# Kernel optimization log

Measured on AMD Instinct MI355X. Metric: run time of the kernel, lower is better.

The kernel has to match this reference:

```python
import jax, jax.numpy as jnp
import numpy as np

T = 464
H = 256  # 256 * network_scale**2 with network_scale=1


def setup_inputs() -> dict:
    key = jax.random.key(0)
    ks = jax.random.split(key, 8)
    B = 64
    feature_encoded = jax.random.normal(ks[0], (B, T, H), dtype=jnp.float32)
    memory_state = jax.random.normal(ks[1], (B, H), dtype=jnp.float32) * 0.1
    carry_state = jax.random.normal(ks[2], (B, H), dtype=jnp.float32) * 0.1
    # LSTM params: kernel [H, 4H], recurrent kernel [H, 4H], bias [4H]; gate order i,f,c,o (Keras)
    # small init scale keeps the relu-activated recurrence numerically stable over 464 steps
    W = jax.random.normal(ks[3], (H, 4 * H), dtype=jnp.float32) * 0.02
    U = jax.random.normal(ks[4], (H, 4 * H), dtype=jnp.float32) * 0.02
    b = jnp.zeros((4 * H,), dtype=jnp.float32)
    # trailing dense: Flatten([B, T, H]) -> Dense(H, relu)
    Wd = jax.random.normal(ks[5], (T * H, H), dtype=jnp.float32) * (1.0 / np.sqrt(T * H))
    bd = jnp.zeros((H,), dtype=jnp.float32)
    return {"feature_encoded": feature_encoded, "memory_state": memory_state,
            "carry_state": carry_state, "W": W, "U": U, "b": b, "Wd": Wd, "bd": bd}


def _lstm_relu(x, h0, c0, W, U, b):
    # Keras LSTM with activation='relu', recurrent_activation='sigmoid'.
    def step(carry, x_t):
        h, c = carry
        z = x_t @ W + h @ U + b           # [B, 4H]
        zi, zf, zg, zo = jnp.split(z, 4, axis=-1)
        i = jax.nn.sigmoid(zi)
        f = jax.nn.sigmoid(zf)
        c = f * c + i * jax.nn.relu(zg)
        o = jax.nn.sigmoid(zo)
        h = o * jax.nn.relu(c)
        return (h, c), h

    xs = jnp.swapaxes(x, 0, 1)            # [T, B, H]
    (hT, cT), ys = jax.lax.scan(step, (h0, c0), xs)
    return jnp.swapaxes(ys, 0, 1), hT, cT  # [B, T, H], [B, H], [B, H]


def reference(feature_encoded, memory_state, carry_state, W, U, b, Wd, bd):
    B = feature_encoded.shape[0]
    x = feature_encoded.reshape(B, T, H)
    seq, hT, cT = _lstm_relu(x, memory_state, carry_state, W, U, b)
    flat = seq.reshape(B, T * H)
    core_output = jax.nn.relu(flat @ Wd + bd)  # [B, H]
    return core_output, hT, cT
```

## Files before the change

### kernel.cpp

```cpp
#include <hip/hip_runtime.h>

#define TT  464
#define HH  256
#define BB  64
#define NWG 64

using bf16x8 = __attribute__((ext_vector_type(8))) short;
using f32x4  = __attribute__((ext_vector_type(4))) float;

__device__ __forceinline__ unsigned short f2bf(float x) {
  union { float f; unsigned u; } v; v.f = x;
  unsigned r = v.u + 0x7fffu + ((v.u >> 16) & 1u);
  return (unsigned short)(r >> 16);
}

__device__ __forceinline__ void wait_flags(int* flags, int base, int target) {
  const int ln  = threadIdx.x & 63;
  int* p = &flags[base + (ln & 31)];
  for (;;) {
    int f = __hip_atomic_load(p, __ATOMIC_RELAXED, __HIP_MEMORY_SCOPE_AGENT);
    if (__all(f >= target)) break;
    __builtin_amdgcn_s_sleep(1);
  }
  asm volatile("" ::: "memory");
}

__global__ __launch_bounds__(256) void lstm_kernel(
    const float* __restrict__ x,
    const float* __restrict__ h0,
    const float* __restrict__ c0,
    const float* __restrict__ W,
    const float* __restrict__ U,
    const float* __restrict__ bias,
    unsigned int* __restrict__ h_bufs,
    unsigned short* __restrict__ seq,
    float* __restrict__ out,
    int* __restrict__ flags)
{
  const int tid = threadIdx.x;
  const int wg  = blockIdx.x;
  const int bgi = wg >> 5;
  const int fgi = wg & 31;
  const int wv  = tid >> 6;
  const int ln  = tid & 63;
  const int mt  = wv >> 1;
  const int nt  = wv & 1;
  const int l15 = ln & 15;
  const int q   = ln >> 4;

  __shared__ unsigned short Bt[32][520];
  __shared__ unsigned short x_lds[32][264];
  __shared__ float          z_lds[32][36];

  for (int it = 0; it < 64; ++it) {
    int i  = it * 256 + tid;
    int k  = i >> 5;
    int n  = i & 31;
    int gc = (n >> 3) * 256 + fgi * 8 + (n & 7);
    float wval = (k < 256) ? W[(size_t)k * 1024 + gc] : U[(size_t)(k - 256) * 1024 + gc];
    Bt[n][k] = f2bf(wval);
  }

  const int r_own = tid >> 3;
  const int j_own = tid & 7;
  const int brow  = bgi * 32 + r_own;
  const int col   = fgi * 8 + j_own;
  float c = c0[brow * HH + col];
  float h = h0[brow * HH + col];
  const float b_i = bias[        col];
  const float b_f = bias[  HH  + col];
  const float b_g = bias[2*HH  + col];
  const float b_o = bias[3*HH  + col];

  {
    unsigned short hb16 = f2bf(h);
    unsigned other = (unsigned)(unsigned short)__shfl_xor((int)hb16, 1);
    if (!(tid & 1)) {
      unsigned hpk = (unsigned)hb16 | (other << 16);
      __hip_atomic_store(&h_bufs[brow * 128 + (col >> 1)], hpk,
                         __ATOMIC_RELAXED, __HIP_MEMORY_SCOPE_AGENT);
    }
  }

  const int xc0  = j_own * 32;
  float4 xr[8];
  {
    const float4* p = (const float4*)(x + ((size_t)brow * TT + 0) * HH + xc0);
#pragma unroll
    for (int i = 0; i < 8; ++i) xr[i] = p[i];
  }

  __builtin_amdgcn_s_waitcnt(0);
  __syncthreads();
  if (tid == 0)
    __hip_atomic_store(&flags[wg], 1, __ATOMIC_RELAXED, __HIP_MEMORY_SCOPE_AGENT);

  for (int t = 0; t < TT; ++t) {
    const int pr  = t & 1;
    const int pwb = pr ^ 1;

    {
      unsigned px[16];
#pragma unroll
      for (int i = 0; i < 8; ++i) {
        px[2*i]   = (unsigned)f2bf(xr[i].x) | ((unsigned)f2bf(xr[i].y) << 16);
        px[2*i+1] = (unsigned)f2bf(xr[i].z) | ((unsigned)f2bf(xr[i].w) << 16);
      }
#pragma unroll
      for (int s = 0; s < 4; ++s) {
        uint4 v = make_uint4(px[4*s], px[4*s+1], px[4*s+2], px[4*s+3]);
        *(uint4*)&x_lds[r_own][xc0 + s * 8] = v;
      }
    }
    {
      const int tn = (t + 1 < TT) ? (t + 1) : (TT - 1);
      const float4* p = (const float4*)(x + ((size_t)brow * TT + tn) * HH + xc0);
#pragma unroll
      for (int i = 0; i < 8; ++i) xr[i] = p[i];
    }

    __syncthreads();

    f32x4 acc = {0.f, 0.f, 0.f, 0.f};
#pragma unroll
    for (int kk = 0; kk < 8; ++kk) {
      bf16x8 afr = *(const bf16x8*)&x_lds[mt * 16 + l15][kk * 32 + q * 8];
      bf16x8 bfr = *(const bf16x8*)&Bt[nt * 16 + l15][kk * 32 + q * 8];
      acc = __builtin_amdgcn_mfma_f32_16x16x32_bf16(afr, bfr, acc, 0, 0, 0);
    }

    wait_flags(flags, bgi * 32, t + 1);

    bf16x8 hf[8];
    {
      const unsigned long long* hb = (const unsigned long long*)h_bufs
          + (size_t)pr * (BB * HH / 4) + (bgi * 32 + mt * 16 + l15) * (HH / 4) + q * 2;
#pragma unroll
      for (int kk = 0; kk < 8; ++kk) {
        union { unsigned long long u[2]; bf16x8 v; } tmp;
        tmp.u[0] = __hip_atomic_load(hb + kk * 8 + 0, __ATOMIC_RELAXED, __HIP_MEMORY_SCOPE_AGENT);
        tmp.u[1] = __hip_atomic_load(hb + kk * 8 + 1, __ATOMIC_RELAXED, __HIP_MEMORY_SCOPE_AGENT);
        hf[kk] = tmp.v;
      }
    }
#pragma unroll
    for (int kk = 0; kk < 8; ++kk) {
      bf16x8 bfr = *(const bf16x8*)&Bt[nt * 16 + l15][256 + kk * 32 + q * 8];
      acc = __builtin_amdgcn_mfma_f32_16x16x32_bf16(hf[kk], bfr, acc, 0, 0, 0);
    }
#pragma unroll
    for (int reg = 0; reg < 4; ++reg)
      z_lds[mt * 16 + q * 4 + reg][nt * 16 + l15] = acc[reg];

    __syncthreads();

    float zi = z_lds[r_own][      j_own] + b_i;
    float zf = z_lds[r_own][ 8 + j_own] + b_f;
    float zg = z_lds[r_own][16 + j_own] + b_g;
    float zo = z_lds[r_own][24 + j_own] + b_o;
    float gi = 1.f / (1.f + __expf(-zi));
    float gf = 1.f / (1.f + __expf(-zf));
    float go = 1.f / (1.f + __expf(-zo));
    float gg = fmaxf(zg, 0.f);
    c = gf * c + gi * gg;
    h = go * fmaxf(c, 0.f);
    unsigned short hb16 = f2bf(h);
    seq[((size_t)brow * TT + t) * HH + col] = hb16;

    {
      unsigned other = (unsigned)(unsigned short)__shfl_xor((int)hb16, 1);
      if (!(tid & 1)) {
        unsigned hpk = (unsigned)hb16 | (other << 16);
        __hip_atomic_store(&h_bufs[pwb * (BB * 128) + brow * 128 + (col >> 1)], hpk,
                           __ATOMIC_RELAXED, __HIP_MEMORY_SCOPE_AGENT);
      }
    }
    __builtin_amdgcn_s_waitcnt(0);
    __syncthreads();
    if (tid == 0)
      __hip_atomic_store(&flags[wg], t + 2, __ATOMIC_RELAXED, __HIP_MEMORY_SCOPE_AGENT);
  }

  out[16384 + brow * HH + col] = h;
  out[32768 + brow * HH + col] = c;
}

#define DP_PA 264
#define DP_PW 258
__global__ __launch_bounds__(256) void dense_partial(
    const unsigned short* __restrict__ seq,
    const float* __restrict__ Wd,
    float* __restrict__ part)
{
  __shared__ __align__(16) char smem[64 * DP_PA * 2];
  unsigned short* a_lds = (unsigned short*)smem;
  float*          Wf    = (float*)smem;

  const int kb  = blockIdx.x;
  const int tid = threadIdx.x;
  const int wv  = tid >> 6;
  const int ln  = tid & 63;
  const int l15 = ln & 15;
  const int q   = ln >> 4;

  f32x4 acc[16];
#pragma unroll
  for (int i = 0; i < 16; ++i) acc[i] = (f32x4){0.f, 0.f, 0.f, 0.f};

  for (int half = 0; half < 2; ++half) {
    const int t = kb + half * 232;
    __syncthreads();
#pragma unroll
    for (int it = 0; it < 8; ++it) {
      int cidx = it * 256 + tid;
      int row  = cidx >> 5;
      int off  = (cidx & 31) * 8;
      *(bf16x8*)&a_lds[row * DP_PA + off] =
          *(const bf16x8*)(seq + ((size_t)row * TT + t) * HH + off);
    }
    __syncthreads();
    bf16x8 af[8];
#pragma unroll
    for (int kk = 0; kk < 8; ++kk)
      af[kk] = *(const bf16x8*)&a_lds[(wv * 16 + l15) * DP_PA + kk * 32 + q * 8];

    for (int ck = 0; ck < 8; ++ck) {
      __syncthreads();
#pragma unroll
      for (int it = 0; it < 8; ++it) {
        int idx = it * 256 + tid;
        int r   = idx >> 6;
        int c4  = (idx & 63) * 4;
        float4 v = *(const float4*)(Wd + ((size_t)(t * 256 + ck * 32 + r)) * HH + c4);
        *(float2*)&Wf[r * DP_PW + c4]     = make_float2(v.x, v.y);
        *(float2*)&Wf[r * DP_PW + c4 + 2] = make_float2(v.z, v.w);
      }
      __syncthreads();
#pragma unroll
      for (int nt2 = 0; nt2 < 16; ++nt2) {
        const int n = nt2 * 16 + l15;
        bf16x8 bfr;
#pragma unroll
        for (int j = 0; j < 8; ++j)
          bfr[j] = (short)f2bf(Wf[(q * 8 + j) * DP_PW + n]);
        acc[nt2] = __builtin_amdgcn_mfma_f32_16x16x32_bf16(af[ck], bfr, acc[nt2], 0, 0, 0);
      }
    }
  }

  float* pb = part + (size_t)kb * (BB * HH);
#pragma unroll
  for (int nt2 = 0; nt2 < 16; ++nt2)
#pragma unroll
    for (int reg = 0; reg < 4; ++reg)
      pb[(wv * 16 + q * 4 + reg) * HH + nt2 * 16 + l15] = acc[nt2][reg];
}

__global__ __launch_bounds__(256) void dense_reduce(
    const float* __restrict__ part,
    const float* __restrict__ bd,
    float* __restrict__ out)
{
  const int o = blockIdx.x * 256 + threadIdx.x;
  float s0 = 0.f, s1 = 0.f, s2 = 0.f, s3 = 0.f;
  for (int kb = 0; kb < 232; kb += 4) {
    s0 += part[(size_t)(kb    ) * 16384 + o];
    s1 += part[(size_t)(kb + 1) * 16384 + o];
    s2 += part[(size_t)(kb + 2) * 16384 + o];
    s3 += part[(size_t)(kb + 3) * 16384 + o];
  }
  float s = (s0 + s1) + (s2 + s3) + bd[o & 255];
  out[o] = fmaxf(s, 0.f);
}

extern "C" void kernel_launch(void* const* d_in, const int* in_sizes, int n_in,
                              void* d_out, int out_size, void* d_ws, size_t ws_size,
                              hipStream_t stream) {
  const float* x  = (const float*)d_in[0];
  const float* h0 = (const float*)d_in[1];
  const float* c0 = (const float*)d_in[2];
  const float* W  = (const float*)d_in[3];
  const float* U  = (const float*)d_in[4];
  const float* bv = (const float*)d_in[5];
  const float* Wd = (const float*)d_in[6];
  const float* bd = (const float*)d_in[7];
  float* out = (float*)d_out;

  char* w = (char*)d_ws;
  int* flags = (int*)w;
  unsigned int*   h_bufs = (unsigned int*)(w + 256);
  unsigned short* seq    = (unsigned short*)(w + 256 + 2 * BB * HH * 2);
  float*          part   = (float*)(w + 256 + 2 * BB * HH * 2 + (size_t)BB * TT * HH * 2);

  hipMemsetAsync(d_ws, 0, 256, stream);
  lstm_kernel<<<NWG, 256, 0, stream>>>(x, h0, c0, W, U, bv, h_bufs, seq, out, flags);
  dense_partial<<<232, 256, 0, stream>>>(seq, Wd, part);
  dense_reduce<<<64, 256, 0, stream>>>(part, bd, out);
}
```

Measured before the change: 2.333 ms.

## Shrink LSTM grid to 8 workgroups with register-resident gate weights

Repartitions the recurrent LSTM kernel from 64 workgroups (32 per batch half) to 8 workgroups (4 per batch half), each owning 64 hidden units across all four gates. Weights are now held in registers, and gate math runs directly on MFMA accumulators, which removes the per-step z_lds shuffle and one barrier. The x tile is double-buffered in LDS. The cross-workgroup flag wait now polls only 4 peers and no longer sleeps, aiming to cut per-step synchronisation latency. The cost is less parallelism per step, with 8x more MFMA work per workgroup, and high register pressure.

After: 3.451 ms. +47.9%, slower.

```diff
diff --git a/kernel.cpp b/kernel.cpp
--- a/kernel.cpp
+++ b/kernel.cpp
@@ -3,7 +3,6 @@
 #define TT  464
 #define HH  256
 #define BB  64
-#define NWG 64
 
 using bf16x8 = __attribute__((ext_vector_type(8))) short;
 using f32x4  = __attribute__((ext_vector_type(4))) float;
@@ -15,17 +14,16 @@
 }
 
 __device__ __forceinline__ void wait_flags(int* flags, int base, int target) {
-  const int ln  = threadIdx.x & 63;
-  int* p = &flags[base + (ln & 31)];
+  const int ln = threadIdx.x & 63;
+  int* p = &flags[base + (ln & 3)];
   for (;;) {
     int f = __hip_atomic_load(p, __ATOMIC_RELAXED, __HIP_MEMORY_SCOPE_AGENT);
     if (__all(f >= target)) break;
-    __builtin_amdgcn_s_sleep(1);
   }
   asm volatile("" ::: "memory");
 }
 
-__global__ __launch_bounds__(256) void lstm_kernel(
+__global__ __launch_bounds__(256, 1) void lstm_kernel(
     const float* __restrict__ x,
     const float* __restrict__ h0,
     const float* __restrict__ c0,
@@ -39,150 +37,198 @@
 {
   const int tid = threadIdx.x;
   const int wg  = blockIdx.x;
-  const int bgi = wg >> 5;
-  const int fgi = wg & 31;
+  const int bgi = wg >> 2;
+  const int ugi = wg & 3;
   const int wv  = tid >> 6;
   const int ln  = tid & 63;
-  const int mt  = wv >> 1;
-  const int nt  = wv & 1;
   const int l15 = ln & 15;
   const int q   = ln >> 4;
 
-  __shared__ unsigned short Bt[32][520];
-  __shared__ unsigned short x_lds[32][264];
-  __shared__ float          z_lds[32][36];
-
-  for (int it = 0; it < 64; ++it) {
-    int i  = it * 256 + tid;
-    int k  = i >> 5;
-    int n  = i & 31;
-    int gc = (n >> 3) * 256 + fgi * 8 + (n & 7);
-    float wval = (k < 256) ? W[(size_t)k * 1024 + gc] : U[(size_t)(k - 256) * 1024 + gc];
-    Bt[n][k] = f2bf(wval);
-  }
+  __shared__ __align__(16) char smem[33792];
+  unsigned short (*Bst)[520]     = (unsigned short(*)[520])smem;
+  unsigned short (*xl)[32][264]  = (unsigned short(*)[32][264])smem;
+
+  bf16x8 wW[4][8], wU[4][8];
+  const int ubase = ugi * 64;
+#pragma unroll
+  for (int g = 0; g < 4; ++g) {
+#pragma unroll
+    for (int half = 0; half < 2; ++half) {
+      __syncthreads();
+      const int cbase = g * 256 + ubase + half * 32;
+      for (int it = 0; it < 64; ++it) {
+        int idx = it * 256 + tid;
+        int k = idx >> 5, n = idx & 31;
+        float val = (k < 256) ? W[(size_t)k * 1024 + cbase + n]
+                              : U[(size_t)(k - 256) * 1024 + cbase + n];
+        Bst[n][k] = f2bf(val);
+      }
+      __syncthreads();
+      if ((wv >> 1) == half) {
+#pragma unroll
+        for (int kk = 0; kk < 8; ++kk) {
+          wW[g][kk] = *(const bf16x8*)&Bst[(wv & 1) * 16 + l15][kk * 32 + q * 8];
+          wU[g][kk] = *(const bf16x8*)&Bst[(wv & 1) * 16 + l15][256 + kk * 32 + q * 8];
+        }
+      }
+    }
+  }
+  __syncthreads();
+
+  const int u   = ubase + wv * 16 + l15;
+  const int rb  = bgi * 32;
+  const float b_i = bias[u], b_f = bias[256 + u], b_g = bias[512 + u], b_o = bias[768 + u];
+  float cst[2][4], hst[2][4];
+#pragma unroll
+  for (int mt = 0; mt < 2; ++mt)
+#pragma unroll
+    for (int r = 0; r < 4; ++r) {
+      int row = rb + mt * 16 + q * 4 + r;
+      cst[mt][r] = c0[row * HH + u];
+      hst[mt][r] = h0[row * HH + u];
+    }
+
+#pragma unroll
+  for (int mt = 0; mt < 2; ++mt)
+#pragma unroll
+    for (int r = 0; r < 4; ++r) {
+      unsigned short hb16 = f2bf(hst[mt][r]);
+      unsigned other = (unsigned)(unsigned short)__shfl_xor((int)hb16, 1);
+      if (!(ln & 1)) {
+        unsigned hpk = (unsigned)hb16 | (other << 16);
+        int row = rb + mt * 16 + q * 4 + r;
+        __hip_atomic_store(&h_bufs[row * 128 + (u >> 1)], hpk,
+                           __ATOMIC_RELAXED, __HIP_MEMORY_SCOPE_AGENT);
+      }
+    }
 
   const int r_own = tid >> 3;
-  const int j_own = tid & 7;
-  const int brow  = bgi * 32 + r_own;
-  const int col   = fgi * 8 + j_own;
-  float c = c0[brow * HH + col];
-  float h = h0[brow * HH + col];
-  const float b_i = bias[        col];
-  const float b_f = bias[  HH  + col];
-  const float b_g = bias[2*HH  + col];
-  const float b_o = bias[3*HH  + col];
-
-  {
-    unsigned short hb16 = f2bf(h);
-    unsigned other = (unsigned)(unsigned short)__shfl_xor((int)hb16, 1);
-    if (!(tid & 1)) {
-      unsigned hpk = (unsigned)hb16 | (other << 16);
-      __hip_atomic_store(&h_bufs[brow * 128 + (col >> 1)], hpk,
-                         __ATOMIC_RELAXED, __HIP_MEMORY_SCOPE_AGENT);
-    }
-  }
-
-  const int xc0  = j_own * 32;
+  const int xc0   = (tid & 7) * 32;
+  const float* xbase = x + (size_t)(rb + r_own) * TT * HH + xc0;
   float4 xr[8];
-  {
-    const float4* p = (const float4*)(x + ((size_t)brow * TT + 0) * HH + xc0);
-#pragma unroll
-    for (int i = 0; i < 8; ++i) xr[i] = p[i];
-  }
+
+  auto stage_x = [&](int buf) {
+    unsigned px[16];
+#pragma unroll
+    for (int i = 0; i < 8; ++i) {
+      px[2*i]   = (unsigned)f2bf(xr[i].x) | ((unsigned)f2bf(xr[i].y) << 16);
+      px[2*i+1] = (unsigned)f2bf(xr[i].z) | ((unsigned)f2bf(xr[i].w) << 16);
+    }
+#pragma unroll
+    for (int s = 0; s < 4; ++s) {
+      uint4 v = make_uint4(px[4*s], px[4*s+1], px[4*s+2], px[4*s+3]);
+      *(uint4*)&xl[buf][r_own][xc0 + s * 8] = v;
+    }
+  };
+
+#pragma unroll
+  for (int i = 0; i < 8; ++i) xr[i] = ((const float4*)xbase)[i];
+  stage_x(0);
+#pragma unroll
+  for (int i = 0; i < 8; ++i) xr[i] = ((const float4*)(xbase + HH))[i];
 
   __builtin_amdgcn_s_waitcnt(0);
   __syncthreads();
   if (tid == 0)
-    __hip_atomic_store(&flags[wg], 1, __ATOMIC_RELAXED, __HIP_MEMORY_SCOPE_AGENT);
+    __hip_atomic_store(&flags[bgi * 16 + ugi], 1, __ATOMIC_RELAXED, __HIP_MEMORY_SCOPE_AGENT);
 
   for (int t = 0; t < TT; ++t) {
     const int pr  = t & 1;
     const int pwb = pr ^ 1;
 
-    {
-      unsigned px[16];
-#pragma unroll
-      for (int i = 0; i < 8; ++i) {
-        px[2*i]   = (unsigned)f2bf(xr[i].x) | ((unsigned)f2bf(xr[i].y) << 16);
-        px[2*i+1] = (unsigned)f2bf(xr[i].z) | ((unsigned)f2bf(xr[i].w) << 16);
-      }
-#pragma unroll
-      for (int s = 0; s < 4; ++s) {
-        uint4 v = make_uint4(px[4*s], px[4*s+1], px[4*s+2], px[4*s+3]);
-        *(uint4*)&x_lds[r_own][xc0 + s * 8] = v;
-      }
-    }
-    {
-      const int tn = (t + 1 < TT) ? (t + 1) : (TT - 1);
-      const float4* p = (const float4*)(x + ((size_t)brow * TT + tn) * HH + xc0);
-#pragma unroll
-      for (int i = 0; i < 8; ++i) xr[i] = p[i];
-    }
-
-    __syncthreads();
-
-    f32x4 acc = {0.f, 0.f, 0.f, 0.f};
-#pragma unroll
-    for (int kk = 0; kk < 8; ++kk) {
-      bf16x8 afr = *(const bf16x8*)&x_lds[mt * 16 + l15][kk * 32 + q * 8];
-      bf16x8 bfr = *(const bf16x8*)&Bt[nt * 16 + l15][kk * 32 + q * 8];
-      acc = __builtin_amdgcn_mfma_f32_16x16x32_bf16(afr, bfr, acc, 0, 0, 0);
-    }
-
-    wait_flags(flags, bgi * 32, t + 1);
-
-    bf16x8 hf[8];
-    {
+    f32x4 acc[2][4];
+#pragma unroll
+    for (int mt = 0; mt < 2; ++mt)
+#pragma unroll
+      for (int g = 0; g < 4; ++g) acc[mt][g] = (f32x4){0.f, 0.f, 0.f, 0.f};
+#pragma unroll
+    for (int mt = 0; mt < 2; ++mt)
+#pragma unroll
+      for (int kk = 0; kk < 8; ++kk) {
+        bf16x8 af = *(const bf16x8*)&xl[pr][mt * 16 + l15][kk * 32 + q * 8];
+#pragma unroll
+        for (int g = 0; g < 4; ++g)
+          acc[mt][g] = __builtin_amdgcn_mfma_f32_16x16x32_bf16(af, wW[g][kk], acc[mt][g], 0, 0, 0);
+      }
+
+    wait_flags(flags, bgi * 16, t + 1);
+
+    bf16x8 hf[2][8];
+#pragma unroll
+    for (int mt = 0; mt < 2; ++mt) {
       const unsigned long long* hb = (const unsigned long long*)h_bufs
-          + (size_t)pr * (BB * HH / 4) + (bgi * 32 + mt * 16 + l15) * (HH / 4) + q * 2;
+          + (size_t)pr * (BB * 64) + (rb + mt * 16 + l15) * 64 + q * 2;
 #pragma unroll
       for (int kk = 0; kk < 8; ++kk) {
-        union { unsigned long long u[2]; bf16x8 v; } tmp;
-        tmp.u[0] = __hip_atomic_load(hb + kk * 8 + 0, __ATOMIC_RELAXED, __HIP_MEMORY_SCOPE_AGENT);
-        tmp.u[1] = __hip_atomic_load(hb + kk * 8 + 1, __ATOMIC_RELAXED, __HIP_MEMORY_SCOPE_AGENT);
-        hf[kk] = tmp.v;
-      }
-    }
-#pragma unroll
-    for (int kk = 0; kk < 8; ++kk) {
-      bf16x8 bfr = *(const bf16x8*)&Bt[nt * 16 + l15][256 + kk * 32 + q * 8];
-      acc = __builtin_amdgcn_mfma_f32_16x16x32_bf16(hf[kk], bfr, acc, 0, 0, 0);
-    }
-#pragma unroll
-    for (int reg = 0; reg < 4; ++reg)
-      z_lds[mt * 16 + q * 4 + reg][nt * 16 + l15] = acc[reg];
-
-    __syncthreads();
-
-    float zi = z_lds[r_own][      j_own] + b_i;
-    float zf = z_lds[r_own][ 8 + j_own] + b_f;
-    float zg = z_lds[r_own][16 + j_own] + b_g;
-    float zo = z_lds[r_own][24 + j_own] + b_o;
-    float gi = 1.f / (1.f + __expf(-zi));
-    float gf = 1.f / (1.f + __expf(-zf));
-    float go = 1.f / (1.f + __expf(-zo));
-    float gg = fmaxf(zg, 0.f);
-    c = gf * c + gi * gg;
-    h = go * fmaxf(c, 0.f);
-    unsigned short hb16 = f2bf(h);
-    seq[((size_t)brow * TT + t) * HH + col] = hb16;
-
-    {
-      unsigned other = (unsigned)(unsigned short)__shfl_xor((int)hb16, 1);
-      if (!(tid & 1)) {
-        unsigned hpk = (unsigned)hb16 | (other << 16);
-        __hip_atomic_store(&h_bufs[pwb * (BB * 128) + brow * 128 + (col >> 1)], hpk,
-                           __ATOMIC_RELAXED, __HIP_MEMORY_SCOPE_AGENT);
-      }
-    }
+        union { unsigned long long uu[2]; bf16x8 v; } tmp;
+        tmp.uu[0] = __hip_atomic_load(hb + kk * 8,     __ATOMIC_RELAXED, __HIP_MEMORY_SCOPE_AGENT);
+        tmp.uu[1] = __hip_atomic_load(hb + kk * 8 + 1, __ATOMIC_RELAXED, __HIP_MEMORY_SCOPE_AGENT);
+        hf[mt][kk] = tmp.v;
+      }
+    }
+#pragma unroll
+    for (int mt = 0; mt < 2; ++mt)
+#pragma unroll
+      for (int kk = 0; kk < 8; ++kk)
+#pragma unroll
+        for (int g = 0; g < 4; ++g)
+          acc[mt][g] = __builtin_amdgcn_mfma_f32_16x16x32_bf16(hf[mt][kk], wU[g][kk], acc[mt][g], 0, 0, 0);
+
+#pragma unroll
+    for (int mt = 0; mt < 2; ++mt)
+#pragma unroll
+      for (int r = 0; r < 4; ++r) {
+        float zi = acc[mt][0][r] + b_i;
+        float zf = acc[mt][1][r] + b_f;
+        float zg = acc[mt][2][r] + b_g;
+        float zo = acc[mt][3][r] + b_o;
+        float gi = __builtin_amdgcn_rcpf(1.f + __expf(-zi));
+        float gf = __builtin_amdgcn_rcpf(1.f + __expf(-zf));
+        float go = __builtin_amdgcn_rcpf(1.f + __expf(-zo));
+        float c  = gf * cst[mt][r] + gi * fmaxf(zg, 0.f);
+        cst[mt][r] = c;
+        hst[mt][r] = go * fmaxf(c, 0.f);
+      }
+
+    stage_x(pwb);
+
+#pragma unroll
+    for (int mt = 0; mt < 2; ++mt)
+#pragma unroll
+      for (int r = 0; r < 4; ++r) {
+        unsigned short hb16 = f2bf(hst[mt][r]);
+        unsigned other = (unsigned)(unsigned short)__shfl_xor((int)hb16, 1);
+        if (!(ln & 1)) {
+          unsigned hpk = (unsigned)hb16 | (other << 16);
+          int row = rb + mt * 16 + q * 4 + r;
+          *(unsigned*)&seq[((size_t)row * TT + t) * HH + u] = hpk;
+          __hip_atomic_store(&h_bufs[pwb * (BB * 128) + row * 128 + (u >> 1)], hpk,
+                             __ATOMIC_RELAXED, __HIP_MEMORY_SCOPE_AGENT);
+        }
+      }
+
     __builtin_amdgcn_s_waitcnt(0);
     __syncthreads();
     if (tid == 0)
-      __hip_atomic_store(&flags[wg], t + 2, __ATOMIC_RELAXED, __HIP_MEMORY_SCOPE_AGENT);
-  }
-
-  out[16384 + brow * HH + col] = h;
-  out[32768 + brow * HH + col] = c;
+      __hip_atomic_store(&flags[bgi * 16 + ugi], t + 2,
+                         __ATOMIC_RELAXED, __HIP_MEMORY_SCOPE_AGENT);
+
+    {
+      const int tn = (t + 2 < TT) ? (t + 2) : (TT - 1);
+      const float4* p = (const float4*)(xbase + (size_t)tn * HH);
+#pragma unroll
+      for (int i = 0; i < 8; ++i) xr[i] = p[i];
+    }
+  }
+
+#pragma unroll
+  for (int mt = 0; mt < 2; ++mt)
+#pragma unroll
+    for (int r = 0; r < 4; ++r) {
+      int row = rb + mt * 16 + q * 4 + r;
+      out[16384 + row * HH + u] = hst[mt][r];
+      out[32768 + row * HH + u] = cst[mt][r];
+    }
 }
 
 #define DP_PA 264
@@ -293,7 +339,7 @@
   float*          part   = (float*)(w + 256 + 2 * BB * HH * 2 + (size_t)BB * TT * HH * 2);
 
   hipMemsetAsync(d_ws, 0, 256, stream);
-  lstm_kernel<<<NWG, 256, 0, stream>>>(x, h0, c0, W, U, bv, h_bufs, seq, out, flags);
+  lstm_kernel<<<8, 256, 0, stream>>>(x, h0, c0, W, U, bv, h_bufs, seq, out, flags);
   dense_partial<<<232, 256, 0, stream>>>(seq, Wd, part);
   dense_reduce<<<64, 256, 0, stream>>>(part, bd, out);
 }
```
